# Kernel optimization log

Hardware: AMD Instinct MI355X
Metric: run time of the kernel (lower is better)

Reference implementation:

```python
import jax, jax.numpy as jnp
import numpy as np

DIM = 8192
BATCH = 8

def setup_inputs() -> dict:
    key = jax.random.key(0)
    k1, k2 = jax.random.split(key)
    sdr = jax.random.normal(k1, (BATCH, DIM), dtype=jnp.float32)
    # scale synapse so sigmoid inputs stay in a reasonable range (weights clamped to [-1,1] in torch)
    synapse = jax.random.normal(k2, (DIM, DIM), dtype=jnp.float32) * (1.0 / np.sqrt(DIM))
    return {"sdr": sdr, "synapse": synapse, "steps": 2, "top_k": 60}

def reference(sdr, synapse, steps, top_k):
    # activation propagation: GEMV/GEMM -> sigmoid -> top-k sparsification per step
    act = sdr.astype(jnp.float32)
    B, N = act.shape
    rows = jnp.arange(B)[:, None]  # [B,1] row indices for scatter
    k = min(int(top_k), N)
    for _ in range(int(steps)):
        act = jax.nn.sigmoid(act @ synapse.T)          # [B,N]
        vals, idx = jax.lax.top_k(act, k)              # [B,k]
        act = jnp.zeros_like(act).at[rows, idx].set(vals)  # keep only top-k activations
    return act
```

## Files before the change

kernel.cpp:

```cpp
#include <hip/hip_runtime.h>
#include <cstdint>


#define DIM 8192
#define BATCH 8
#define KSPLIT 4
#define KSPAN 2048
#define ROWS_PER_BLK 64
#define GEMV_THREADS 512
#define ROWS_PER_WAVE 8

__device__ __forceinline__ float sigmoidf_(float x) {
    return 1.0f / (1.0f + __expf(-x));
}

__global__ __launch_bounds__(GEMV_THREADS) void gemv_part(
    const float* __restrict__ A,
    const float* __restrict__ W,
    float* __restrict__ P)
{
    __shared__ float As[BATCH * KSPAN];

    const int tid     = threadIdx.x;
    const int h       = blockIdx.x & 3;
    const int rowbase = (blockIdx.x >> 2) * ROWS_PER_BLK;
    const int kbeg    = h * KSPAN;

    {
        const float4* Ag  = (const float4*)A;
        float4*       As4 = (float4*)As;
#pragma unroll
        for (int i = 0; i < 8; ++i) {
            const int q = tid + i * GEMV_THREADS;
            const int b = q >> 9;
            const int c = q & 511;
            As4[q] = Ag[b * (DIM / 4) + (kbeg >> 2) + c];
        }
    }
    __syncthreads();

    const int lane = tid & 63;
    const int wid  = tid >> 6;

    for (int t = 0; t < ROWS_PER_WAVE; ++t) {
        const int r = rowbase + wid * ROWS_PER_WAVE + t;
        const float* wr = W + (size_t)r * DIM + kbeg + lane * 4;

        float4 w[8];
#pragma unroll
        for (int win = 0; win < 8; ++win)
            w[win] = *(const float4*)(wr + win * 256);

        float acc[8];
#pragma unroll
        for (int b = 0; b < 8; ++b) acc[b] = 0.0f;

#pragma unroll
        for (int win = 0; win < 8; ++win) {
            const float* abase = As + win * 256 + lane * 4;
#pragma unroll
            for (int b = 0; b < 8; ++b) {
                const float4 a = *(const float4*)(abase + b * KSPAN);
                acc[b] += w[win].x * a.x;
                acc[b] += w[win].y * a.y;
                acc[b] += w[win].z * a.z;
                acc[b] += w[win].w * a.w;
            }
        }

#pragma unroll
        for (int b = 0; b < 8; ++b) {
            float v = acc[b];
#pragma unroll
            for (int off = 32; off > 0; off >>= 1)
                v += __shfl_down(v, off, 64);
            if (lane == 0)
                P[((size_t)(h * BATCH + b)) * DIM + r] = v;
        }
    }
}


__device__ __forceinline__ void scan_small(const int* hist, int nb, int k_need,
                                           int lane, int* s_cut, int* s_gt)
{
    int running = 0;
    for (int cb = nb - 64; cb >= 0; cb -= 64) {
        const int b = cb + 63 - lane;
        const int val = hist[b];
        int c = val;
#pragma unroll
        for (int o = 1; o < 64; o <<= 1) {
            const int u = __shfl_up(c, o, 64);
            if (lane >= o) c += u;
        }
        const unsigned long long m = __ballot(running + c >= k_need);
        if (m) {
            const int f = (int)__ffsll(m) - 1;
            const int cf = __shfl(c, f, 64);
            const int vf = __shfl(val, f, 64);
            if (lane == 0) { *s_cut = cb + 63 - f; *s_gt = running + cf - vf; }
            return;
        }
        running += __shfl(c, 63, 64);
    }
    if (lane == 0) { *s_cut = 0; *s_gt = 0; }
}

__device__ __forceinline__ void scan_l1(const int* hist, const int* coarse,
                                        int k_need, int lane,
                                        int* s_cut, int* s_gt)
{
    int running = 0, seg = -1, segGT = 0;
    for (int cb = 192; cb >= 0 && seg < 0; cb -= 64) {
        const int b = cb + 63 - lane;
        const int val = coarse[b];
        int c = val;
#pragma unroll
        for (int o = 1; o < 64; o <<= 1) {
            const int u = __shfl_up(c, o, 64);
            if (lane >= o) c += u;
        }
        const unsigned long long m = __ballot(running + c >= k_need);
        if (m) {
            const int f = (int)__ffsll(m) - 1;
            seg = cb + 63 - f;
            segGT = running + __shfl(c, f, 64) - __shfl(val, f, 64);
        } else {
            running += __shfl(c, 63, 64);
        }
    }
    if (seg < 0) seg = 0;
    const int b = seg * 32 + 31 - lane;
    const int val = (lane < 32) ? hist[b] : 0;
    int c = val;
#pragma unroll
    for (int o = 1; o < 64; o <<= 1) {
        const int u = __shfl_up(c, o, 64);
        if (lane >= o) c += u;
    }
    const unsigned long long m = __ballot(segGT + c >= k_need);
    const int f = (int)__ffsll(m) - 1;
    const int cf = __shfl(c, f, 64);
    const int vf = __shfl(val, f, 64);
    if (lane == 0) { *s_cut = seg * 32 + 31 - f; *s_gt = segGT + cf - vf; }
}

__global__ __launch_bounds__(256) void topk_fused(
    const float* __restrict__ P,
    float* __restrict__ Yout,
    const int* __restrict__ kptr)
{
    const int row  = blockIdx.x;
    const int tid  = threadIdx.x;
    const int lane = tid & 63;
    const int wid  = tid >> 6;
    int k = kptr ? *kptr : 60;
    if (k > DIM) k = DIM;

    uint32_t v[32];
    const float* Pb = P + (size_t)row * DIM;
#pragma unroll
    for (int i = 0; i < 32; ++i) {
        const int idx = tid + i * 256;
        float s = Pb[idx];
        s += Pb[idx + 1 * BATCH * DIM];
        s += Pb[idx + 2 * BATCH * DIM];
        s += Pb[idx + 3 * BATCH * DIM];
        v[i] = __float_as_uint(sigmoidf_(s));
    }

    float* dst = Yout + (size_t)row * DIM;
    if (k <= 0) {
#pragma unroll
        for (int i = 0; i < 32; ++i) dst[tid + i * 256] = 0.0f;
        return;
    }

    __shared__ int hist[8192];
    __shared__ int coarse[256];
    __shared__ int s_cut, s_gt, s_ctr;

    for (int i = tid; i < 8192; i += 256) hist[i] = 0;
    __syncthreads();
#pragma unroll
    for (int i = 0; i < 32; ++i) atomicAdd(&hist[v[i] >> 17], 1);
    __syncthreads();
    {
        int s = 0;
        const int base = tid * 32;
        for (int i = 0; i < 32; ++i) s += hist[base + i];
        coarse[tid] = s;
    }
    __syncthreads();
    if (wid == 0) scan_l1(hist, coarse, k, lane, &s_cut, &s_gt);
    __syncthreads();
    const uint32_t cut1 = (uint32_t)s_cut;
    const int gt1 = s_gt;

    for (int i = tid; i < 512; i += 256) hist[i] = 0;
    __syncthreads();
#pragma unroll
    for (int i = 0; i < 32; ++i)
        if ((v[i] >> 17) == cut1) atomicAdd(&hist[(v[i] >> 8) & 0x1FF], 1);
    __syncthreads();
    if (wid == 0) scan_small(hist, 512, k - gt1, lane, &s_cut, &s_gt);
    __syncthreads();
    const uint32_t cut2 = (uint32_t)s_cut;
    const int gt2 = s_gt;

    const uint32_t pref = (cut1 << 9) | cut2;
    for (int i = tid; i < 256; i += 256) hist[i] = 0;
    if (tid == 0) s_ctr = 0;
    __syncthreads();
#pragma unroll
    for (int i = 0; i < 32; ++i)
        if ((v[i] >> 8) == pref) atomicAdd(&hist[v[i] & 0xFF], 1);
    __syncthreads();
    if (wid == 0) scan_small(hist, 256, k - gt1 - gt2, lane, &s_cut, &s_gt);
    __syncthreads();
    const uint32_t cut3 = (uint32_t)s_cut;
    const int gt3 = s_gt;

    const uint32_t cutoff  = (pref << 8) | cut3;
    const int      need_eq = k - (gt1 + gt2 + gt3);

#pragma unroll
    for (int i = 0; i < 32; ++i) {
        const uint32_t b = v[i];
        float val = 0.0f;
        if (b > cutoff) {
            val = __uint_as_float(b);
        } else if (b == cutoff) {
            const int pos = atomicAdd(&s_ctr, 1);
            if (pos < need_eq) val = __uint_as_float(b);
        }
        dst[tid + i * 256] = val;
    }
}

extern "C" void kernel_launch(void* const* d_in, const int* in_sizes, int n_in,
                              void* d_out, int out_size, void* d_ws, size_t ws_size,
                              hipStream_t stream) {
    const float* sdr = (const float*)d_in[0];
    const float* syn = (const float*)d_in[1];
    const int* kptr  = (n_in > 3) ? (const int*)d_in[3] : nullptr;
    float* out = (float*)d_out;
    float* P   = (float*)d_ws;

    const int nblk = KSPLIT * (DIM / ROWS_PER_BLK);

    gemv_part<<<nblk, GEMV_THREADS, 0, stream>>>(sdr, syn, P);
    topk_fused<<<8, 256, 0, stream>>>(P, out, kptr);
    gemv_part<<<nblk, GEMV_THREADS, 0, stream>>>(out, syn, P);
    topk_fused<<<8, 256, 0, stream>>>(P, out, kptr);
}
```

Measured before the change: 568.3 us.

## Interleave four weight rows per wave with prefetched float4 windows in GEMV

```diff
diff --git a/kernel.cpp b/kernel.cpp
--- a/kernel.cpp
+++ b/kernel.cpp
@@ -6,15 +6,15 @@
 #define BATCH 8
 #define KSPLIT 4
 #define KSPAN 2048
-#define ROWS_PER_BLK 64
+#define ROWS_PER_BLK 32
 #define GEMV_THREADS 512
-#define ROWS_PER_WAVE 8
+#define ROWS_PER_WAVE 4
 
 __device__ __forceinline__ float sigmoidf_(float x) {
     return 1.0f / (1.0f + __expf(-x));
 }
 
-__global__ __launch_bounds__(GEMV_THREADS) void gemv_part(
+__global__ __launch_bounds__(GEMV_THREADS, 4) void gemv_part(
     const float* __restrict__ A,
     const float* __restrict__ W,
     float* __restrict__ P)
@@ -41,41 +41,62 @@
 
     const int lane = tid & 63;
     const int wid  = tid >> 6;
-
-    for (int t = 0; t < ROWS_PER_WAVE; ++t) {
-        const int r = rowbase + wid * ROWS_PER_WAVE + t;
-        const float* wr = W + (size_t)r * DIM + kbeg + lane * 4;
-
-        float4 w[8];
-#pragma unroll
-        for (int win = 0; win < 8; ++win)
-            w[win] = *(const float4*)(wr + win * 256);
-
-        float acc[8];
-#pragma unroll
-        for (int b = 0; b < 8; ++b) acc[b] = 0.0f;
-
-#pragma unroll
-        for (int win = 0; win < 8; ++win) {
+    const int r0   = rowbase + wid * ROWS_PER_WAVE;
+
+    const float* wr[ROWS_PER_WAVE];
+#pragma unroll
+    for (int r = 0; r < ROWS_PER_WAVE; ++r)
+        wr[r] = W + (size_t)(r0 + r) * DIM + kbeg + lane * 4;
+
+    float acc[ROWS_PER_WAVE][8];
+#pragma unroll
+    for (int r = 0; r < ROWS_PER_WAVE; ++r)
+#pragma unroll
+        for (int b = 0; b < 8; ++b) acc[r][b] = 0.0f;
+
+    float4 wc[ROWS_PER_WAVE], wn[ROWS_PER_WAVE];
+#pragma unroll
+    for (int r = 0; r < ROWS_PER_WAVE; ++r)
+        wc[r] = *(const float4*)(wr[r]);
+
+#pragma unroll
+    for (int win = 0; win < 8; ++win) {
+        if (win < 7) {
+#pragma unroll
+            for (int r = 0; r < ROWS_PER_WAVE; ++r)
+                wn[r] = *(const float4*)(wr[r] + (win + 1) * 256);
+        }
+        float4 a[8];
+        {
             const float* abase = As + win * 256 + lane * 4;
 #pragma unroll
+            for (int b = 0; b < 8; ++b)
+                a[b] = *(const float4*)(abase + b * KSPAN);
+        }
+#pragma unroll
+        for (int r = 0; r < ROWS_PER_WAVE; ++r) {
+#pragma unroll
             for (int b = 0; b < 8; ++b) {
-                const float4 a = *(const float4*)(abase + b * KSPAN);
-                acc[b] += w[win].x * a.x;
-                acc[b] += w[win].y * a.y;
-                acc[b] += w[win].z * a.z;
-                acc[b] += w[win].w * a.w;
+                acc[r][b] += wc[r].x * a[b].x;
+                acc[r][b] += wc[r].y * a[b].y;
+                acc[r][b] += wc[r].z * a[b].z;
+                acc[r][b] += wc[r].w * a[b].w;
             }
         }
-
+#pragma unroll
+        for (int r = 0; r < ROWS_PER_WAVE; ++r) wc[r] = wn[r];
+    }
+
+#pragma unroll
+    for (int r = 0; r < ROWS_PER_WAVE; ++r) {
 #pragma unroll
         for (int b = 0; b < 8; ++b) {
-            float v = acc[b];
+            float v = acc[r][b];
 #pragma unroll
             for (int off = 32; off > 0; off >>= 1)
                 v += __shfl_down(v, off, 64);
             if (lane == 0)
-                P[((size_t)(h * BATCH + b)) * DIM + r] = v;
+                P[((size_t)(h * BATCH + b)) * DIM + (r0 + r)] = v;
         }
     }
 }
```

Result: slower. 1.332 ms (+134.4%).
